# Kernel tuning notes

Hardware: AMD Instinct MI355X
Metric: run time of the kernel (lower is better)

The kernel has to match this reference:

```python
import jax, jax.numpy as jnp
import numpy as np

B, N, F, C = 8, 256, 59, 128
BOX = 20.0
EPS = 1e-5


def _bn(y, g, b, m, v):
    # eval-mode BatchNorm1d over the channel (last) axis
    return (y - m) * jax.lax.rsqrt(v + EPS) * g + b


def setup_inputs() -> dict:
    key = jax.random.key(0)
    ks = jax.random.split(key, 12)
    x = jax.random.normal(ks[0], (B, N, F), jnp.float32)
    pos = jax.random.uniform(ks[1], (B, N, 3), jnp.float32) * BOX
    nrm = jax.random.normal(ks[2], (B, N, 3), jnp.float32)
    normal = nrm / jnp.linalg.norm(nrm, axis=-1, keepdims=True)
    s_in = 1.0 / np.sqrt(F)
    W_lin = jax.random.normal(ks[3], (C, F), jnp.float32) * s_in
    W_src = jax.random.normal(ks[4], (C, F), jnp.float32) * s_in
    W_dst = jax.random.normal(ks[5], (C, F), jnp.float32) * s_in
    pos_w = jax.random.normal(ks[6], (C, 6), jnp.float32) * (1.0 / np.sqrt(6.0))
    pos_b = jax.random.normal(ks[7], (C,), jnp.float32) * 0.02
    attn_w = jax.random.normal(ks[8], (C, C), jnp.float32) * (1.0 / np.sqrt(C))
    attn_b = jax.random.normal(ks[9], (C,), jnp.float32) * 0.02
    pos_bn_g = 1.0 + 0.1 * jax.random.normal(ks[10], (C,), jnp.float32)
    attn_bn_g = 1.0 + 0.1 * jax.random.normal(ks[11], (C,), jnp.float32)
    zeros = jnp.zeros((C,), jnp.float32)
    ones = jnp.ones((C,), jnp.float32)
    return {
        'x': x, 'pos': pos, 'normal': normal,
        'W_lin': W_lin, 'W_src': W_src, 'W_dst': W_dst,
        'pos_w': pos_w, 'pos_b': pos_b,
        'pos_bn_g': pos_bn_g, 'pos_bn_b': zeros, 'pos_bn_m': zeros, 'pos_bn_v': ones,
        'attn_w': attn_w, 'attn_b': attn_b,
        'attn_bn_g': attn_bn_g, 'attn_bn_b': zeros, 'attn_bn_m': zeros, 'attn_bn_v': ones,
        'r': 5,
    }


def reference(x, pos, normal, W_lin, W_src, W_dst, pos_w, pos_b,
              pos_bn_g, pos_bn_b, pos_bn_m, pos_bn_v,
              attn_w, attn_b, attn_bn_g, attn_bn_b, attn_bn_m, attn_bn_v, r):
    r = jnp.float32(r)
    # linear projections (bias-free, as in PyG PointTransformerConv)
    v = jnp.einsum('bnf,cf->bnc', x, W_lin)      # values
    a_src = jnp.einsum('bnf,cf->bnc', x, W_src)  # alpha for source j
    a_dst = jnp.einsum('bnf,cf->bnc', x, W_dst)  # alpha for dest   i
    # relative geometry, axis 1 = receiver i, axis 2 = sender j
    rel_pos = pos[:, :, None, :] - pos[:, None, :, :]          # [B,i,j,3]
    rel_nrm = normal[:, :, None, :] - normal[:, None, :, :]    # [B,i,j,3]
    relf = jnp.concatenate([rel_pos, rel_nrm], axis=-1)        # [B,i,j,6]
    # pos_nn = Linear(6,C) + BN + ReLU (eval)
    delta = jax.nn.relu(_bn(jnp.einsum('bijk,ck->bijc', relf, pos_w) + pos_b,
                            pos_bn_g, pos_bn_b, pos_bn_m, pos_bn_v))
    # attn_nn(alpha_i - alpha_j + delta)
    alpha_arg = a_dst[:, :, None, :] - a_src[:, None, :, :] + delta
    scores = jax.nn.relu(_bn(jnp.einsum('bijc,dc->bijd', alpha_arg, attn_w) + attn_b,
                             attn_bn_g, attn_bn_b, attn_bn_m, attn_bn_v))
    # radius mask within each graph (self-loops included, dist 0 <= r)
    dist2 = jnp.sum(rel_pos * rel_pos, axis=-1)                # [B,i,j]
    mask = (dist2 <= r * r)[..., None]                         # [B,i,j,1]
    attn = jax.nn.softmax(jnp.where(mask, scores, -jnp.inf), axis=2)
    # per-channel vector attention over neighbors j: sum_j attn * (v_j + delta)
    out = jnp.sum(attn * (v[:, None, :, :] + delta), axis=2)   # [B,i,C]
    return out
```

## Files before the change

kernel.cpp:

```cpp
#include <hip/hip_runtime.h>

typedef _Float16 h2 __attribute__((ext_vector_type(2)));
typedef _Float16 f16x8 __attribute__((ext_vector_type(8)));
typedef float f32x4 __attribute__((ext_vector_type(4)));
typedef unsigned int uint32;

#define BB 8
#define NN 256
#define FF 59
#define CC 128
#define EPSV 1e-5f

#define WS_V     0
#define WS_ASRC  (WS_V + BB*NN*CC)
#define WS_ADST  (WS_ASRC + BB*NN*CC)
#define WS_PWT   (WS_ADST + BB*NN*CC)
#define WS_T1    (WS_PWT + 6*CC)
#define WS_T2    (WS_T1 + CC)
#define WS_WTB   (WS_T2 + CC)

__global__ __launch_bounds__(256) void prep_kernel(
    const float* __restrict__ x, const float* __restrict__ W_lin,
    const float* __restrict__ W_src, const float* __restrict__ W_dst,
    const float* __restrict__ pos_w, const float* __restrict__ pos_b,
    const float* __restrict__ pos_g, const float* __restrict__ pos_bb,
    const float* __restrict__ pos_m, const float* __restrict__ pos_v,
    const float* __restrict__ attn_w, const float* __restrict__ attn_b,
    const float* __restrict__ attn_g, const float* __restrict__ attn_bb,
    const float* __restrict__ attn_m, const float* __restrict__ attn_v,
    float* __restrict__ ws)
{
    int blk = blockIdx.x;
    int tid = threadIdx.x;
    if (blk < 768) {
        int type = blk >> 8;
        int g    = blk & 255;
        int b    = g >> 5;
        int n0   = (g & 31) * 8;
        const float* W = (type == 0) ? W_lin : (type == 1) ? W_src : W_dst;
        float* outp = ws + ((type == 0) ? WS_V : (type == 1) ? WS_ASRC : WS_ADST);
        __shared__ float Wl[CC * 60];
        __shared__ float xs[8 * 60];
        for (int idx = tid; idx < CC * 60; idx += 256) {
            int r = idx / 60, f = idx - r * 60;
            Wl[idx] = (f < FF) ? W[r * FF + f] : 0.f;
        }
        const float* xrow = x + (size_t)(b * NN + n0) * FF;
        for (int idx = tid; idx < 8 * 60; idx += 256) {
            int r = idx / 60, f = idx - r * 60;
            xs[idx] = (f < FF) ? xrow[r * FF + f] : 0.f;
        }
        __syncthreads();
        int c = tid & 127, h = tid >> 7;
        float acc[4];
#pragma unroll
        for (int q = 0; q < 4; ++q) acc[q] = 0.f;
#pragma unroll 3
        for (int f4 = 0; f4 < 15; ++f4) {
            float4 wq = *(const float4*)&Wl[c * 60 + f4 * 4];
#pragma unroll
            for (int q = 0; q < 4; ++q) {
                float4 xq = *(const float4*)&xs[(h * 4 + q) * 60 + f4 * 4];
                acc[q] = fmaf(wq.x, xq.x, acc[q]);
                acc[q] = fmaf(wq.y, xq.y, acc[q]);
                acc[q] = fmaf(wq.z, xq.z, acc[q]);
                acc[q] = fmaf(wq.w, xq.w, acc[q]);
            }
        }
#pragma unroll
        for (int q = 0; q < 4; ++q) {
            int n = n0 + h * 4 + q;
            outp[(b * NN + n) * CC + c] = acc[q];
        }
    } else {
        __shared__ float S2s[CC];
        if (tid < CC) {
            int c = tid;
            float S1 = rsqrtf(pos_v[c] + EPSV) * pos_g[c];
            ws[WS_T1 + c] = (pos_b[c] - pos_m[c]) * S1 + pos_bb[c];
#pragma unroll
            for (int k = 0; k < 6; ++k) ws[WS_PWT + k * CC + c] = pos_w[c * 6 + k] * S1;
            float S2 = rsqrtf(attn_v[c] + EPSV) * attn_g[c];
            S2s[c] = S2;
            ws[WS_T2 + c] = (attn_b[c] - attn_m[c]) * S2 + attn_bb[c];
        }
        __syncthreads();
        uint4* wtbp = (uint4*)(ws + WS_WTB);
        for (int idx = tid; idx < 32 * 64; idx += 256) {
            int l = idx & 63, ts = idx >> 6;
            int t = ts >> 2, s = ts & 3;
            int d  = t * 16 + (l & 15);
            int c0 = s * 32 + ((l >> 4) << 3);
            float S2 = S2s[d];
            float4 w0 = *(const float4*)&attn_w[d * CC + c0];
            float4 w1 = *(const float4*)&attn_w[d * CC + c0 + 4];
            h2 p0, p1, p2, p3;
            p0.x = (_Float16)(w0.x * S2); p0.y = (_Float16)(w0.y * S2);
            p1.x = (_Float16)(w0.z * S2); p1.y = (_Float16)(w0.w * S2);
            p2.x = (_Float16)(w1.x * S2); p2.y = (_Float16)(w1.y * S2);
            p3.x = (_Float16)(w1.z * S2); p3.y = (_Float16)(w1.w * S2);
            uint4 o;
            o.x = __builtin_bit_cast(uint32, p0);
            o.y = __builtin_bit_cast(uint32, p1);
            o.z = __builtin_bit_cast(uint32, p2);
            o.w = __builtin_bit_cast(uint32, p3);
            wtbp[idx] = o;
        }
    }
}

__global__ __launch_bounds__(256, 4) void main_kernel(
    const float* __restrict__ pos, const float* __restrict__ nrm,
    const int* __restrict__ rptr, const float* __restrict__ ws,
    float* __restrict__ out)
{
    const float* v    = ws + WS_V;
    const float* asrc = ws + WS_ASRC;
    const float* adst = ws + WS_ADST;
    const float* pwt  = ws + WS_PWT;
    const float* T1   = ws + WS_T1;
    const float* T2   = ws + WS_T2;

    int blk = blockIdx.x;
    int b = blk >> 8, i = blk & 255;
    int tid = threadIdx.x;

    __shared__ float relf[NN * 6];
    __shared__ int   jlist[NN];
    __shared__ int   wcnt[4];
    __shared__ int   cnt_s;
    __shared__ _Float16 alpha_h[16 * 136];
    __shared__ float    u_lds[16 * 136];

    int rv = rptr[0];
    float r2 = (float)(rv * rv);
    const float* pib = pos + (size_t)(b * NN + i) * 3;
    const float* nib = nrm + (size_t)(b * NN + i) * 3;
    float pix = pib[0], piy = pib[1], piz = pib[2];
    float nix = nib[0], niy = nib[1], niz = nib[2];
    {
        int j = tid;
        const float* pj = pos + (size_t)(b * NN + j) * 3;
        const float* nj = nrm + (size_t)(b * NN + j) * 3;
        float dx = pix - pj[0], dy = piy - pj[1], dz = piz - pj[2];
        float ex = nix - nj[0], ey = niy - nj[1], ez = niz - nj[2];
        float d2 = dx * dx + dy * dy + dz * dz;
        bool valid = (d2 <= r2);
        unsigned long long m = __ballot(valid);
        int w = tid >> 6, lane = tid & 63;
        if (lane == 0) wcnt[w] = __popcll(m);
        __syncthreads();
        int off = 0;
        for (int w2 = 0; w2 < w; ++w2) off += wcnt[w2];
        if (tid == 0) cnt_s = wcnt[0] + wcnt[1] + wcnt[2] + wcnt[3];
        int rank = __popcll(m & ((1ull << lane) - 1ull));
        if (valid) {
            int s = off + rank;
            jlist[s] = j;
            relf[s * 6 + 0] = dx; relf[s * 6 + 1] = dy; relf[s * 6 + 2] = dz;
            relf[s * 6 + 3] = ex; relf[s * 6 + 4] = ey; relf[s * 6 + 5] = ez;
        }
    }
    __syncthreads();
    int cnt = cnt_s;

    int c    = tid & 127;
    int half = tid >> 7;
    int w    = tid >> 6;
    int lane = tid & 63;

    f16x8 bf[2][4];
    {
        const uint4* wtb = (const uint4*)(ws + WS_WTB);
#pragma unroll
        for (int tt = 0; tt < 2; ++tt)
#pragma unroll
            for (int s = 0; s < 4; ++s)
                bf[tt][s] = __builtin_bit_cast(f16x8,
                    wtb[((w * 2 + tt) * 4 + s) * 64 + lane]);
    }
    float T2a = T2[w * 32 + (lane & 15)];
    float T2b = T2[w * 32 + 16 + (lane & 15)];

    float pw[6];
#pragma unroll
    for (int k = 0; k < 6; ++k) pw[k] = pwt[k * CC + c];
    float T1c    = T1[c];
    float adst_c = adst[(b * NN + i) * CC + c];

    float pse0 = 0.f, pov0 = 0.f, pse1 = 0.f, pov1 = 0.f;

    for (int base = 0; base < cnt; base += 16) {
        int tcnt = min(16, cnt - base);
        int myn  = tcnt - half * 8;
#pragma unroll
        for (int q = 0; q < 8; ++q) {
            float aval = 0.f, uval = 0.f;
            if (q < myn) {
                int js = base + half * 8 + q;
                int j  = jlist[js];
                const float2* rp = (const float2*)&relf[js * 6];
                float2 r0 = rp[0], r1 = rp[1], r2f = rp[2];
                float dsum = T1c;
                dsum = fmaf(pw[0], r0.x, dsum);
                dsum = fmaf(pw[1], r0.y, dsum);
                dsum = fmaf(pw[2], r1.x, dsum);
                dsum = fmaf(pw[3], r1.y, dsum);
                dsum = fmaf(pw[4], r2f.x, dsum);
                dsum = fmaf(pw[5], r2f.y, dsum);
                float delta = fmaxf(dsum, 0.f);
                aval = adst_c - asrc[(b * NN + j) * CC + c] + delta;
                uval = v[(b * NN + j) * CC + c] + delta;
            }
            alpha_h[(half * 8 + q) * 136 + c] = (_Float16)aval;
            u_lds[(half * 8 + q) * 136 + c]  = uval;
        }
        __syncthreads();
        f32x4 acc0 = {T2a, T2a, T2a, T2a};
        f32x4 acc1 = {T2b, T2b, T2b, T2b};
        {
            const _Float16* arow = &alpha_h[(lane & 15) * 136 + ((lane >> 4) << 3)];
#pragma unroll
            for (int s = 0; s < 4; ++s) {
                f16x8 af = *(const f16x8*)(arow + s * 32);
                acc0 = __builtin_amdgcn_mfma_f32_16x16x32_f16(af, bf[0][s], acc0, 0, 0, 0);
                acc1 = __builtin_amdgcn_mfma_f32_16x16x32_f16(af, bf[1][s], acc1, 0, 0, 0);
            }
        }
        {
            int d0 = w * 32 + (lane & 15);
#pragma unroll
            for (int rg = 0; rg < 4; ++rg) {
                int j = ((lane >> 4) << 2) + rg;
                bool jvalid = (j < tcnt);
                float e0 = jvalid ? __expf(fmaxf(acc0[rg], 0.f)) : 0.f;
                float e1 = jvalid ? __expf(fmaxf(acc1[rg], 0.f)) : 0.f;
                pse0 += e0;
                pov0 += e0 * u_lds[j * 136 + d0];
                pse1 += e1;
                pov1 += e1 * u_lds[j * 136 + d0 + 16];
            }
        }
        __syncthreads();
    }

    pse0 += __shfl_xor(pse0, 16); pse0 += __shfl_xor(pse0, 32);
    pov0 += __shfl_xor(pov0, 16); pov0 += __shfl_xor(pov0, 32);
    pse1 += __shfl_xor(pse1, 16); pse1 += __shfl_xor(pse1, 32);
    pov1 += __shfl_xor(pov1, 16); pov1 += __shfl_xor(pov1, 32);
    if (lane < 16) {
        size_t o = (size_t)(b * NN + i) * CC + w * 32 + lane;
        out[o]      = pov0 / pse0;
        out[o + 16] = pov1 / pse1;
    }
}

extern "C" void kernel_launch(void* const* d_in, const int* in_sizes, int n_in,
                              void* d_out, int out_size, void* d_ws, size_t ws_size,
                              hipStream_t stream) {
    const float* x      = (const float*)d_in[0];
    const float* pos    = (const float*)d_in[1];
    const float* normal = (const float*)d_in[2];
    const float* W_lin  = (const float*)d_in[3];
    const float* W_src  = (const float*)d_in[4];
    const float* W_dst  = (const float*)d_in[5];
    const float* pos_w  = (const float*)d_in[6];
    const float* pos_b  = (const float*)d_in[7];
    const float* pos_g  = (const float*)d_in[8];
    const float* pos_bb = (const float*)d_in[9];
    const float* pos_m  = (const float*)d_in[10];
    const float* pos_v  = (const float*)d_in[11];
    const float* attn_w = (const float*)d_in[12];
    const float* attn_b = (const float*)d_in[13];
    const float* attn_g = (const float*)d_in[14];
    const float* attn_bb= (const float*)d_in[15];
    const float* attn_m = (const float*)d_in[16];
    const float* attn_v = (const float*)d_in[17];
    const int*   rptr   = (const int*)d_in[18];
    float* ws  = (float*)d_ws;
    float* out = (float*)d_out;

    prep_kernel<<<dim3(769), dim3(256), 0, stream>>>(
        x, W_lin, W_src, W_dst, pos_w, pos_b, pos_g, pos_bb, pos_m, pos_v,
        attn_w, attn_b, attn_g, attn_bb, attn_m, attn_v, ws);
    main_kernel<<<dim3(2048), dim3(256), 0, stream>>>(pos, normal, rptr, ws, out);
}
```

Measured before the change: 114.6 us.

## Hoist weight loads, balance neighbor slots, and transpose W layout in LDS

The attention kernel now issues its MFMA weight, T1/T2, pos-weight and a_dst loads before the radius neighbor search, so their latency overlaps the ballot/compaction phase. Neighbor slots are interleaved between the two thread halves, which evens out the work when the last tile is partial. Zero-filling of unused tile rows is dropped, and the trailing barrier becomes a conditional barrier at the top of the loop; rows past tcnt may then hold stale data, but they are masked out in the softmax stage. In the prep kernel, W is stored in LDS as f4-major float4 rows indexed by channel, which removes the stride-60 access pattern when each thread reads its weights.

New measurement: 113.2 us. About the same (-1.3%).

```diff
diff --git a/kernel.cpp b/kernel.cpp
--- a/kernel.cpp
+++ b/kernel.cpp
@@ -39,11 +39,17 @@
         int n0   = (g & 31) * 8;
         const float* W = (type == 0) ? W_lin : (type == 1) ? W_src : W_dst;
         float* outp = ws + ((type == 0) ? WS_V : (type == 1) ? WS_ASRC : WS_ADST);
-        __shared__ float Wl[CC * 60];
+        __shared__ float Wl[15 * 128 * 4];
         __shared__ float xs[8 * 60];
-        for (int idx = tid; idx < CC * 60; idx += 256) {
-            int r = idx / 60, f = idx - r * 60;
-            Wl[idx] = (f < FF) ? W[r * FF + f] : 0.f;
+        for (int idx = tid; idx < 15 * 128; idx += 256) {
+            int f4 = idx >> 7, cc = idx & 127;
+            const float* wr = W + cc * FF + f4 * 4;
+            float4 wv;
+            wv.x = wr[0];
+            wv.y = wr[1];
+            wv.z = wr[2];
+            wv.w = (f4 < 14) ? wr[3] : 0.f;
+            *(float4*)&Wl[idx * 4] = wv;
         }
         const float* xrow = x + (size_t)(b * NN + n0) * FF;
         for (int idx = tid; idx < 8 * 60; idx += 256) {
@@ -57,7 +63,7 @@
         for (int q = 0; q < 4; ++q) acc[q] = 0.f;
 #pragma unroll 3
         for (int f4 = 0; f4 < 15; ++f4) {
-            float4 wq = *(const float4*)&Wl[c * 60 + f4 * 4];
+            float4 wq = *(const float4*)&Wl[(f4 * 128 + c) * 4];
 #pragma unroll
             for (int q = 0; q < 4; ++q) {
                 float4 xq = *(const float4*)&xs[(h * 4 + q) * 60 + f4 * 4];
@@ -132,6 +138,29 @@
     __shared__ _Float16 alpha_h[16 * 136];
     __shared__ float    u_lds[16 * 136];
 
+    int c    = tid & 127;
+    int half = tid >> 7;
+    int w    = tid >> 6;
+    int lane = tid & 63;
+
+    f16x8 bf[2][4];
+    {
+        const uint4* wtb = (const uint4*)(ws + WS_WTB);
+#pragma unroll
+        for (int tt = 0; tt < 2; ++tt)
+#pragma unroll
+            for (int s = 0; s < 4; ++s)
+                bf[tt][s] = __builtin_bit_cast(f16x8,
+                    wtb[((w * 2 + tt) * 4 + s) * 64 + lane]);
+    }
+    float T2a = T2[w * 32 + (lane & 15)];
+    float T2b = T2[w * 32 + 16 + (lane & 15)];
+    float pw[6];
+#pragma unroll
+    for (int k = 0; k < 6; ++k) pw[k] = pwt[k * CC + c];
+    float T1c    = T1[c];
+    float adst_c = adst[(b * NN + i) * CC + c];
+
     int rv = rptr[0];
     float r2 = (float)(rv * rv);
     const float* pib = pos + (size_t)(b * NN + i) * 3;
@@ -147,7 +176,6 @@
         float d2 = dx * dx + dy * dy + dz * dz;
         bool valid = (d2 <= r2);
         unsigned long long m = __ballot(valid);
-        int w = tid >> 6, lane = tid & 63;
         if (lane == 0) wcnt[w] = __popcll(m);
         __syncthreads();
         int off = 0;
@@ -164,40 +192,16 @@
     __syncthreads();
     int cnt = cnt_s;
 
-    int c    = tid & 127;
-    int half = tid >> 7;
-    int w    = tid >> 6;
-    int lane = tid & 63;
-
-    f16x8 bf[2][4];
-    {
-        const uint4* wtb = (const uint4*)(ws + WS_WTB);
-#pragma unroll
-        for (int tt = 0; tt < 2; ++tt)
-#pragma unroll
-            for (int s = 0; s < 4; ++s)
-                bf[tt][s] = __builtin_bit_cast(f16x8,
-                    wtb[((w * 2 + tt) * 4 + s) * 64 + lane]);
-    }
-    float T2a = T2[w * 32 + (lane & 15)];
-    float T2b = T2[w * 32 + 16 + (lane & 15)];
-
-    float pw[6];
-#pragma unroll
-    for (int k = 0; k < 6; ++k) pw[k] = pwt[k * CC + c];
-    float T1c    = T1[c];
-    float adst_c = adst[(b * NN + i) * CC + c];
-
     float pse0 = 0.f, pov0 = 0.f, pse1 = 0.f, pov1 = 0.f;
 
     for (int base = 0; base < cnt; base += 16) {
+        if (base) __syncthreads();
         int tcnt = min(16, cnt - base);
-        int myn  = tcnt - half * 8;
 #pragma unroll
         for (int q = 0; q < 8; ++q) {
-            float aval = 0.f, uval = 0.f;
-            if (q < myn) {
-                int js = base + half * 8 + q;
+            int s = 2 * q + half;
+            if (s < tcnt) {
+                int js = base + s;
                 int j  = jlist[js];
                 const float2* rp = (const float2*)&relf[js * 6];
                 float2 r0 = rp[0], r1 = rp[1], r2f = rp[2];
@@ -209,11 +213,9 @@
                 dsum = fmaf(pw[4], r2f.x, dsum);
                 dsum = fmaf(pw[5], r2f.y, dsum);
                 float delta = fmaxf(dsum, 0.f);
-                aval = adst_c - asrc[(b * NN + j) * CC + c] + delta;
-                uval = v[(b * NN + j) * CC + c] + delta;
-            }
-            alpha_h[(half * 8 + q) * 136 + c] = (_Float16)aval;
-            u_lds[(half * 8 + q) * 136 + c]  = uval;
+                alpha_h[s * 136 + c] = (_Float16)(adst_c - asrc[(b * NN + j) * CC + c] + delta);
+                u_lds[s * 136 + c]   = v[(b * NN + j) * CC + c] + delta;
+            }
         }
         __syncthreads();
         f32x4 acc0 = {T2a, T2a, T2a, T2a};
@@ -232,16 +234,16 @@
 #pragma unroll
             for (int rg = 0; rg < 4; ++rg) {
                 int j = ((lane >> 4) << 2) + rg;
-                bool jvalid = (j < tcnt);
-                float e0 = jvalid ? __expf(fmaxf(acc0[rg], 0.f)) : 0.f;
-                float e1 = jvalid ? __expf(fmaxf(acc1[rg], 0.f)) : 0.f;
-                pse0 += e0;
-                pov0 += e0 * u_lds[j * 136 + d0];
-                pse1 += e1;
-                pov1 += e1 * u_lds[j * 136 + d0 + 16];
-            }
-        }
-        __syncthreads();
+                if (j < tcnt) {
+                    float e0 = __expf(fmaxf(acc0[rg], 0.f));
+                    float e1 = __expf(fmaxf(acc1[rg], 0.f));
+                    pse0 += e0;
+                    pov0 += e0 * u_lds[j * 136 + d0];
+                    pse1 += e1;
+                    pov1 += e1 * u_lds[j * 136 + d0 + 16];
+                }
+            }
+        }
     }
 
     pse0 += __shfl_xor(pse0, 16); pse0 += __shfl_xor(pse0, 32);
```
